# Kernel optimization log

Measured on AMD Instinct MI355X. Metric: run time of the kernel, lower is better.

Reference implementation:

```python
import jax, jax.numpy as jnp
import numpy as np

B, L, E = 4, 2048, 1024
H, D = E // 64, 64
FF = E // 4 * 11  # 2816

def _ln(x, g, b, eps=1e-5):
    m = jnp.mean(x, axis=-1, keepdims=True)
    v = jnp.mean((x - m) ** 2, axis=-1, keepdims=True)
    return (x - m) * jax.lax.rsqrt(v + eps) * g + b

def _fwd(x, g_norm, b_norm, W_ffn1, b_ffn1, W_ffn2, b_ffn2, g_head, b_head, mem,
         g_mem, b_mem, W_q, b_q, W_k, b_k, W_v, b_v, W_g, b_g, W_mg, b_mg,
         W_o, b_o, W_op, b_op, g_ctx, b_ctx, seq_dim):
    # Pre-norm + FFN (SiLU MLP), residual
    x_norm = _ln(x, g_norm, b_norm)
    x_mlp = x + jax.nn.silu(x_norm @ W_ffn1 + b_ffn1) @ W_ffn2 + b_ffn2
    # causal cumsum gating per head
    xc = jnp.cumsum(x_mlp, axis=seq_dim)
    x_h = x_mlp.reshape(B, L, H, D)
    xc_h = xc.reshape(B, L, H, D)
    align = jnp.sum(_ln(x_h, g_head, b_head) * _ln(xc_h, g_head, b_head),
                    axis=-1, keepdims=True) / (D ** 0.5)
    context = jnp.cumsum((x_h * jax.nn.sigmoid(align)).reshape(B, L, E), axis=seq_dim)
    # delta-rule fast-weight memory
    ctx = _ln(x_mlp + context, g_mem, b_mem)
    q = ctx @ W_q + b_q
    k = ctx @ W_k + b_k
    k = k / jnp.maximum(jnp.linalg.norm(k, axis=-1, keepdims=True), 1e-5)  # F.normalize
    v = ctx @ W_v + b_v
    gate = jax.nn.sigmoid(ctx @ W_g + b_g)
    prev = jnp.broadcast_to(mem, (B, E, E))
    scale = E ** 0.5
    v_ret = jnp.einsum('ble,bef->blf', k, prev) / scale
    v_dyn = gate * (v - v_ret)
    mem_out_prev = jnp.einsum('ble,bef->blf', q, prev)
    scores_causal = jnp.einsum('bld,bmd->blm', q, k) * jnp.tril(jnp.ones((L, L), q.dtype))
    mem_out = (mem_out_prev + jnp.einsum('blm,bmf->blf', scores_causal, v_dyn) / scale) / scale
    out = jax.nn.silu(mem_out @ W_o + b_o) @ W_op + b_op
    y = x_mlp + _ln(out, g_ctx, b_ctx)
    return y, scores_causal

def setup_inputs():
    key = jax.random.key(0)
    ks = jax.random.split(key, 12)
    w = lambda k, s: (jax.random.normal(k, s) * 0.02).astype(jnp.float32)
    z = lambda s: jnp.zeros(s, jnp.float32)
    o = lambda s: jnp.ones(s, jnp.float32)
    return {
        'x': jax.random.normal(ks[0], (B, L, E), jnp.float32),
        'g_norm': o((E,)), 'b_norm': z((E,)),
        'W_ffn1': w(ks[1], (E, FF)), 'b_ffn1': z((FF,)),
        'W_ffn2': w(ks[2], (FF, E)), 'b_ffn2': z((E,)),
        'g_head': o((D,)), 'b_head': z((D,)),
        'mem': w(ks[3], (1, E, E)),
        'g_mem': o((E,)), 'b_mem': z((E,)),
        'W_q': w(ks[4], (E, E)), 'b_q': z((E,)),
        'W_k': w(ks[5], (E, E)), 'b_k': z((E,)),
        'W_v': w(ks[6], (E, E)), 'b_v': z((E,)),
        'W_g': w(ks[7], (E, E)), 'b_g': z((E,)),
        'W_mg': w(ks[8], (E, E)), 'b_mg': z((E,)),
        'W_o': w(ks[9], (E, 4 * E)), 'b_o': z((4 * E,)),
        'W_op': w(ks[10], (4 * E, E)), 'b_op': z((E,)),
        'g_ctx': o((E,)), 'b_ctx': z((E,)),
        'seq_dim': 1,
    }

def reference(x, g_norm, b_norm, W_ffn1, b_ffn1, W_ffn2, b_ffn2, g_head, b_head, mem,
              g_mem, b_mem, W_q, b_q, W_k, b_k, W_v, b_v, W_g, b_g, W_mg, b_mg,
              W_o, b_o, W_op, b_op, g_ctx, b_ctx, seq_dim):
    return _fwd(x, g_norm, b_norm, W_ffn1, b_ffn1, W_ffn2, b_ffn2, g_head, b_head, mem,
                g_mem, b_mem, W_q, b_q, W_k, b_k, W_v, b_v, W_g, b_g, W_mg, b_mg,
                W_o, b_o, W_op, b_op, g_ctx, b_ctx, seq_dim)
```

## Files before the change

### kernel.cpp

```cpp
#include <hip/hip_runtime.h>
#include <math.h>

#define B_ 4
#define L_ 2048
#define E_ 1024
#define H_ 16
#define D_ 64
#define FF_ 2816
#define M_ (B_*L_)
#define E4_ 4096
#define CH_ 64
#define NC_ (L_/CH_)

typedef unsigned short ushort_t;
typedef __attribute__((ext_vector_type(8))) short short8;
typedef __attribute__((ext_vector_type(4))) float f32x4;
typedef __attribute__((ext_vector_type(4))) unsigned short ushort4v;

__device__ inline ushort_t f2b(float x) {
  union { float f; unsigned u; } v; v.f = x;
  unsigned r = v.u + 0x7FFFu + ((v.u >> 16) & 1u);
  return (ushort_t)(r >> 16);
}
__device__ inline float b2f(ushort_t h) {
  union { unsigned u; float f; } v; v.u = ((unsigned)h) << 16; return v.f;
}
__device__ inline void split8(const float* s, short8& hi, short8& lo) {
#pragma unroll
  for (int i = 0; i < 8; ++i) {
    unsigned u; { union { float f; unsigned x; } c; c.f = s[i]; u = c.x; }
    unsigned hu = u & 0xFFFF0000u;
    hi[i] = (short)(hu >> 16);
    union { unsigned x; float f; } hc; hc.x = hu;
    lo[i] = (short)f2b(s[i] - hc.f);
  }
}

__device__ inline float wave_sum(float a) {
#pragma unroll
  for (int off = 1; off < 64; off <<= 1) a += __shfl_xor(a, off);
  return a;
}
__device__ inline void wave_reduce2(float& a, float& b) {
#pragma unroll
  for (int off = 1; off < 64; off <<= 1) {
    a += __shfl_xor(a, off);
    b += __shfl_xor(b, off);
  }
}

__global__ __launch_bounds__(256) void ln_rows(
    const float* __restrict__ in, const float* __restrict__ g,
    const float* __restrict__ bb, const float* __restrict__ res_after,
    float* __restrict__ outf, ushort_t* __restrict__ outb,
    ushort_t* __restrict__ outbl)
{
  int row = blockIdx.x;
  int t = threadIdx.x;
  float4 v = ((const float4*)(in + (size_t)row * E_))[t];
  float s = wave_sum(v.x + v.y + v.z + v.w);
  __shared__ float ra[4], rb[4];
  int w = t >> 6;
  if ((t & 63) == 0) ra[w] = s;
  __syncthreads();
  float mean = (ra[0] + ra[1] + ra[2] + ra[3]) * (1.f / E_);
  float dx = v.x - mean, dy = v.y - mean, dz = v.z - mean, dw = v.w - mean;
  float s2 = wave_sum(dx*dx + dy*dy + dz*dz + dw*dw);
  if ((t & 63) == 0) rb[w] = s2;
  __syncthreads();
  float var = (rb[0] + rb[1] + rb[2] + rb[3]) * (1.f / E_);
  float r = rsqrtf(var + 1e-5f);
  float4 gv = ((const float4*)g)[t];
  float4 bv = ((const float4*)bb)[t];
  float4 o;
  o.x = dx * r * gv.x + bv.x;
  o.y = dy * r * gv.y + bv.y;
  o.z = dz * r * gv.z + bv.z;
  o.w = dw * r * gv.w + bv.w;
  if (res_after) {
    float4 rv = ((const float4*)(res_after + (size_t)row * E_))[t];
    o.x += rv.x; o.y += rv.y; o.z += rv.z; o.w += rv.w;
  }
  if (outf) ((float4*)(outf + (size_t)row * E_))[t] = o;
  if (outb) {
    ushort4v hb; hb.x = f2b(o.x); hb.y = f2b(o.y); hb.z = f2b(o.z); hb.w = f2b(o.w);
    *(ushort4v*)(outb + (size_t)row * E_ + t * 4) = hb;
    if (outbl) {
      ushort4v lb;
      lb.x = f2b(o.x - b2f(hb.x)); lb.y = f2b(o.y - b2f(hb.y));
      lb.z = f2b(o.z - b2f(hb.z)); lb.w = f2b(o.w - b2f(hb.w));
      *(ushort4v*)(outbl + (size_t)row * E_ + t * 4) = lb;
    }
  }
}

__global__ __launch_bounds__(256) void knorm_rows(
    const float* __restrict__ kin, ushort_t* __restrict__ kh,
    ushort_t* __restrict__ kl)
{
  int row = blockIdx.x;
  int t = threadIdx.x;
  float4 v = ((const float4*)(kin + (size_t)row * E_))[t];
  float s2 = wave_sum(v.x*v.x + v.y*v.y + v.z*v.z + v.w*v.w);
  __shared__ float rb2[4];
  int w = t >> 6;
  if ((t & 63) == 0) rb2[w] = s2;
  __syncthreads();
  s2 = rb2[0] + rb2[1] + rb2[2] + rb2[3];
  float sc = 1.f / fmaxf(sqrtf(s2), 1e-5f);
  float f0 = v.x * sc, f1 = v.y * sc, f2 = v.z * sc, f3 = v.w * sc;
  ushort4v hb; hb.x = f2b(f0); hb.y = f2b(f1); hb.z = f2b(f2); hb.w = f2b(f3);
  ushort4v lb;
  lb.x = f2b(f0 - b2f(hb.x)); lb.y = f2b(f1 - b2f(hb.y));
  lb.z = f2b(f2 - b2f(hb.z)); lb.w = f2b(f3 - b2f(hb.w));
  *(ushort4v*)(kh + (size_t)row * E_ + t * 4) = hb;
  *(ushort4v*)(kl + (size_t)row * E_ + t * 4) = lb;
}

__global__ __launch_bounds__(256) void chunk_partials(
    const float* __restrict__ x, float* __restrict__ S)
{
  int c = blockIdx.x, b = blockIdx.y, t = threadIdx.x;
  const float4* xp = (const float4*)(x + ((size_t)b * L_ + (size_t)c * CH_) * E_);
  float4 acc = make_float4(0.f, 0.f, 0.f, 0.f);
  for (int l = 0; l < CH_; ++l) {
    float4 v = xp[(size_t)l * (E_/4) + t];
    acc.x += v.x; acc.y += v.y; acc.z += v.z; acc.w += v.w;
  }
  ((float4*)(S + ((size_t)b * NC_ + c) * E_))[t] = acc;
}

__global__ __launch_bounds__(256) void scan_partials(float* __restrict__ S)
{
  int b = blockIdx.x, t = threadIdx.x;
  float4 run = make_float4(0.f, 0.f, 0.f, 0.f);
  for (int c = 0; c < NC_; ++c) {
    float4* p = (float4*)(S + ((size_t)b * NC_ + c) * E_);
    float4 v = p[t];
    p[t] = run;
    run.x += v.x; run.y += v.y; run.z += v.z; run.w += v.w;
  }
}

__global__ __launch_bounds__(64) void align_gate(
    const float* __restrict__ xmlp, const float* __restrict__ Sx,
    const float* __restrict__ gh, const float* __restrict__ bh,
    float* __restrict__ gated, float* __restrict__ G)
{
  int c = blockIdx.x, h = blockIdx.y, b = blockIdx.z;
  int d = threadIdx.x;
  int e = h * D_ + d;
  float xc = Sx[((size_t)b * NC_ + c) * E_ + e];
  float gsum = 0.f;
  float ghd = gh[d], bhd = bh[d];
  const float* xp = xmlp + ((size_t)b * L_ + (size_t)c * CH_) * E_ + e;
  float* gp = gated + ((size_t)b * L_ + (size_t)c * CH_) * E_ + e;
  for (int l = 0; l < CH_; ++l) {
    float xv = xp[(size_t)l * E_];
    xc += xv;
    float sx = xv, sc = xc;
    wave_reduce2(sx, sc);
    float mx = sx * (1.f/64.f), mc = sc * (1.f/64.f);
    float dx = xv - mx, dc = xc - mc;
    float vx = dx * dx, vc = dc * dc;
    wave_reduce2(vx, vc);
    vx *= (1.f/64.f); vc *= (1.f/64.f);
    float nx  = dx * rsqrtf(vx + 1e-5f) * ghd + bhd;
    float ncv = dc * rsqrtf(vc + 1e-5f) * ghd + bhd;
    float dotv = wave_sum(nx * ncv);
    float align = dotv * 0.125f;
    float sig = 1.f / (1.f + expf(-align));
    float gv = xv * sig;
    gp[(size_t)l * E_] = gv;
    gsum += gv;
  }
  G[((size_t)b * NC_ + c) * E_ + e] = gsum;
}

__global__ __launch_bounds__(256) void context_add(
    const float* __restrict__ gated, const float* __restrict__ Gx,
    const float* __restrict__ xmlp, float* __restrict__ t_out)
{
  int c = blockIdx.x, b = blockIdx.y, t = threadIdx.x;
  float4 run = ((const float4*)(Gx + ((size_t)b * NC_ + c) * E_))[t];
  size_t base = ((size_t)b * L_ + (size_t)c * CH_) * (E_/4);
  const float4* gp = (const float4*)gated;
  const float4* xp = (const float4*)xmlp;
  float4* op = (float4*)t_out;
  for (int l = 0; l < CH_; ++l) {
    size_t idx = base + (size_t)l * (E_/4) + t;
    float4 g = gp[idx];
    run.x += g.x; run.y += g.y; run.z += g.z; run.w += g.w;
    float4 x = xp[idx];
    float4 o;
    o.x = x.x + run.x; o.y = x.y + run.y; o.z = x.z + run.z; o.w = x.w + run.w;
    op[idx] = o;
  }
}

__global__ __launch_bounds__(256) void wcvt_t(
    const float* __restrict__ in, ushort_t* __restrict__ outh,
    ushort_t* __restrict__ outl, int R, int C)
{
  __shared__ float t[32][33];
  int c0 = blockIdx.x * 32, r0 = blockIdx.y * 32;
  int tid = threadIdx.x;
  int r = tid >> 3, c4 = (tid & 7) * 4;
  float4 v = *(const float4*)(in + (size_t)(r0 + r) * C + c0 + c4);
  t[r][c4] = v.x; t[r][c4+1] = v.y; t[r][c4+2] = v.z; t[r][c4+3] = v.w;
  __syncthreads();
  int c = tid >> 3, r4 = (tid & 7) * 4;
  float f0 = t[r4][c], f1 = t[r4+1][c], f2 = t[r4+2][c], f3 = t[r4+3][c];
  ushort4v hb; hb.x = f2b(f0); hb.y = f2b(f1); hb.z = f2b(f2); hb.w = f2b(f3);
  *(ushort4v*)(outh + (size_t)(c0 + c) * R + r0 + r4) = hb;
  if (outl) {
    ushort4v lb;
    lb.x = f2b(f0 - b2f(hb.x)); lb.y = f2b(f1 - b2f(hb.y));
    lb.z = f2b(f2 - b2f(hb.z)); lb.w = f2b(f3 - b2f(hb.w));
    *(ushort4v*)(outl + (size_t)(c0 + c) * R + r0 + r4) = lb;
  }
}

__global__ __launch_bounds__(256) void tpose_f32(
    const float* __restrict__ in, float* __restrict__ out)
{
  __shared__ float t[32][33];
  int b = blockIdx.z;
  const float* ib = in + (size_t)b * L_ * E_;
  float* ob = out + (size_t)b * E_ * L_;
  int c0 = blockIdx.x * 32, r0 = blockIdx.y * 32;
  int tid = threadIdx.x;
  int r = tid >> 3, c4 = (tid & 7) * 4;
  float4 v = *(const float4*)(ib + (size_t)(r0 + r) * E_ + c0 + c4);
  t[r][c4] = v.x; t[r][c4+1] = v.y; t[r][c4+2] = v.z; t[r][c4+3] = v.w;
  __syncthreads();
  int c = tid >> 3, r4 = (tid & 7) * 4;
  float4 o;
  o.x = t[r4][c]; o.y = t[r4+1][c]; o.z = t[r4+2][c]; o.w = t[r4+3][c];
  *(float4*)(ob + (size_t)(c0 + c) * L_ + r0 + r4) = o;
}

enum { EPI_PLAIN = 0, EPI_BIAS = 1, EPI_SILU = 2, EPI_SIG = 3,
       EPI_BIAS_RES = 4, EPI_VDYN = 5, EPI_PV = 6, EPI_TRIL = 7, EPI_RES = 8 };

struct GemmP {
  const ushort_t *A, *Al, *Bt, *Btl;
  const float *Af, *Btf;
  float* Cf; ushort_t *Cb, *Cbl;
  int N, K, ldA, ldB;
  long long sA, sB, sCf, sCb, sRes, sAux;
  const float *bias, *res, *aux;
  int epi, causal;
};

template <int MODE>
__global__ __launch_bounds__(256) void gemm_k(GemmP p)
{
  __shared__ __align__(16) short As[4][2][128][8];
  __shared__ __align__(16) short Bs[4][2][128][8];

  int z = blockIdx.z;
  int row0 = blockIdx.y * 128, col0 = blockIdx.x * 128;
  int tid = threadIdx.x;

  if (p.causal == 1 && col0 > row0) {
    float* Cf = p.Cf ? p.Cf + (size_t)z * p.sCf : nullptr;
    float4 zf = make_float4(0.f, 0.f, 0.f, 0.f);
#pragma unroll
    for (int i = 0; i < 16; ++i) {
      int e4 = tid + 256 * i;
      int r = e4 >> 5, c4 = (e4 & 31) * 4;
      if (Cf) *(float4*)(Cf + (size_t)(row0 + r) * p.N + col0 + c4) = zf;
    }
    return;
  }

  int lane = tid & 63, wave = tid >> 6;
  int wm = wave >> 1, wn = wave & 1;
  int lr = lane & 15, kq = lane >> 4;
  int lrx = lr ^ (kq << 1);

  int kend = p.K;
  if (p.causal == 2) { int ke = row0 + 128; kend = ke < p.K ? ke : p.K; }

  int kw = tid & 3, m0 = tid >> 2, m1 = m0 + 64;
  int sl0 = m0 ^ (kw << 1), sl1 = m1 ^ (kw << 1);

  size_t aoff0 = (size_t)(row0 + m0) * p.ldA + kw * 8;
  size_t aoff1 = (size_t)(row0 + m1) * p.ldA + kw * 8;
  size_t boff0 = (size_t)(col0 + m0) * p.ldB + kw * 8;
  size_t boff1 = (size_t)(col0 + m1) * p.ldB + kw * 8;

  const ushort_t *Ah = nullptr, *Bh = nullptr, *Alo = nullptr, *Blo = nullptr;
  const float *Af = nullptr, *Bf = nullptr;
  if constexpr (MODE == 2) {
    Af = p.Af  + (size_t)z * p.sA;
    Bf = p.Btf + (size_t)z * p.sB;
  } else {
    Ah = p.A  + (size_t)z * p.sA;
    Bh = p.Bt + (size_t)z * p.sB;
    if constexpr (MODE == 1) {
      Alo = p.Al  + (size_t)z * p.sA;
      Blo = p.Btl + (size_t)z * p.sB;
    }
  }

  f32x4 acc[4][4] = {};

  short8 a0h, a1h, b0h, b1h, a0l, a1l, b0l, b1l;
  float fa0[8], fa1[8], fb0[8], fb1[8];

  if constexpr (MODE == 2) {
    *(float4*)&fa0[0] = *(const float4*)(Af + aoff0);
    *(float4*)&fa0[4] = *(const float4*)(Af + aoff0 + 4);
    *(float4*)&fa1[0] = *(const float4*)(Af + aoff1);
    *(float4*)&fa1[4] = *(const float4*)(Af + aoff1 + 4);
    *(float4*)&fb0[0] = *(const float4*)(Bf + boff0);
    *(float4*)&fb0[4] = *(const float4*)(Bf + boff0 + 4);
    *(float4*)&fb1[0] = *(const float4*)(Bf + boff1);
    *(float4*)&fb1[4] = *(const float4*)(Bf + boff1 + 4);
  } else {
    a0h = *(const short8*)(Ah + aoff0);
    a1h = *(const short8*)(Ah + aoff1);
    b0h = *(const short8*)(Bh + boff0);
    b1h = *(const short8*)(Bh + boff1);
    if constexpr (MODE == 1) {
      a0l = *(const short8*)(Alo + aoff0);
      a1l = *(const short8*)(Alo + aoff1);
      b0l = *(const short8*)(Blo + boff0);
      b1l = *(const short8*)(Blo + boff1);
    }
  }

  for (int k0 = 0; k0 < kend; k0 += 32) {
    __syncthreads();
    if constexpr (MODE == 2) {
      split8(fa0, a0h, a0l); split8(fa1, a1h, a1l);
      split8(fb0, b0h, b0l); split8(fb1, b1h, b1l);
    }
    *(short8*)&As[kw][0][sl0][0] = a0h;
    *(short8*)&As[kw][0][sl1][0] = a1h;
    *(short8*)&Bs[kw][0][sl0][0] = b0h;
    *(short8*)&Bs[kw][0][sl1][0] = b1h;
    if constexpr (MODE != 0) {
      *(short8*)&As[kw][1][sl0][0] = a0l;
      *(short8*)&As[kw][1][sl1][0] = a1l;
      *(short8*)&Bs[kw][1][sl0][0] = b0l;
      *(short8*)&Bs[kw][1][sl1][0] = b1l;
    }
    __syncthreads();
    if (k0 + 32 < kend) {
      size_t kk = k0 + 32;
      if constexpr (MODE == 2) {
        *(float4*)&fa0[0] = *(const float4*)(Af + aoff0 + kk);
        *(float4*)&fa0[4] = *(const float4*)(Af + aoff0 + kk + 4);
        *(float4*)&fa1[0] = *(const float4*)(Af + aoff1 + kk);
        *(float4*)&fa1[4] = *(const float4*)(Af + aoff1 + kk + 4);
        *(float4*)&fb0[0] = *(const float4*)(Bf + boff0 + kk);
        *(float4*)&fb0[4] = *(const float4*)(Bf + boff0 + kk + 4);
        *(float4*)&fb1[0] = *(const float4*)(Bf + boff1 + kk);
        *(float4*)&fb1[4] = *(const float4*)(Bf + boff1 + kk + 4);
      } else {
        a0h = *(const short8*)(Ah + aoff0 + kk);
        a1h = *(const short8*)(Ah + aoff1 + kk);
        b0h = *(const short8*)(Bh + boff0 + kk);
        b1h = *(const short8*)(Bh + boff1 + kk);
        if constexpr (MODE == 1) {
          a0l = *(const short8*)(Alo + aoff0 + kk);
          a1l = *(const short8*)(Alo + aoff1 + kk);
          b0l = *(const short8*)(Blo + boff0 + kk);
          b1l = *(const short8*)(Blo + boff1 + kk);
        }
      }
    }
    short8 bh[4], bl[4];
#pragma unroll
    for (int ni = 0; ni < 4; ++ni) {
      bh[ni] = *(const short8*)&Bs[kq][0][wn * 64 + ni * 16 + lrx][0];
      if (MODE != 0) bl[ni] = *(const short8*)&Bs[kq][1][wn * 64 + ni * 16 + lrx][0];
    }
#pragma unroll
    for (int mi = 0; mi < 4; ++mi) {
      short8 ah = *(const short8*)&As[kq][0][wm * 64 + mi * 16 + lrx][0];
      short8 alv;
      if (MODE != 0) alv = *(const short8*)&As[kq][1][wm * 64 + mi * 16 + lrx][0];
#pragma unroll
      for (int ni = 0; ni < 4; ++ni) {
        acc[mi][ni] = __builtin_amdgcn_mfma_f32_16x16x32_bf16(
            ah, bh[ni], acc[mi][ni], 0, 0, 0);
        if (MODE != 0) {
          acc[mi][ni] = __builtin_amdgcn_mfma_f32_16x16x32_bf16(
              alv, bh[ni], acc[mi][ni], 0, 0, 0);
          acc[mi][ni] = __builtin_amdgcn_mfma_f32_16x16x32_bf16(
              ah, bl[ni], acc[mi][ni], 0, 0, 0);
        }
      }
    }
  }

  float* Cf = p.Cf ? p.Cf + (size_t)z * p.sCf : nullptr;
  ushort_t* Cb  = p.Cb  ? p.Cb  + (size_t)z * p.sCb : nullptr;
  ushort_t* Cbl = p.Cbl ? p.Cbl + (size_t)z * p.sCb : nullptr;
  const float* res = p.res ? p.res + (size_t)z * p.sRes : nullptr;
  const float* aux = p.aux ? p.aux + (size_t)z * p.sAux : nullptr;
  const float INV32 = 0.03125f;
  int rbase = kq * 4;

#pragma unroll
  for (int mi = 0; mi < 4; ++mi) {
#pragma unroll
    for (int r = 0; r < 4; ++r) {
      int grow = row0 + wm * 64 + mi * 16 + rbase + r;
      size_t rowoff = (size_t)grow * p.N;
#pragma unroll
      for (int ni = 0; ni < 4; ++ni) {
        int gcol = col0 + wn * 64 + ni * 16 + lr;
        size_t idx = rowoff + gcol;
        float v = acc[mi][ni][r];
        switch (p.epi) {
          case EPI_PLAIN: break;
          case EPI_BIAS: v += p.bias[gcol]; break;
          case EPI_SILU: v += p.bias[gcol]; v = v / (1.f + expf(-v)); break;
          case EPI_SIG:  v = 1.f / (1.f + expf(-(v + p.bias[gcol]))); break;
          case EPI_BIAS_RES: v += p.bias[gcol] + res[idx]; break;
          case EPI_VDYN: v = aux[idx] * (res[idx] - v * INV32); break;
          case EPI_PV:   v = (res[idx] + v * INV32) * INV32; break;
          case EPI_TRIL: v = (gcol <= grow) ? v : 0.f; break;
          case EPI_RES:  v += res[idx]; break;
        }
        if (Cf) Cf[idx] = v;
        if (Cb) {
          ushort_t hi = f2b(v);
          Cb[idx] = hi;
          if (Cbl) Cbl[idx] = f2b(v - b2f(hi));
        }
      }
    }
  }
}

struct GArgs {
  int mode;
  const ushort_t *A, *Al, *Bt, *Btl;
  const float *Af, *Btf;
  float* Cf; ushort_t *Cb, *Cbl;
  int M, N, K, ldA, ldB, nb;
  long long sA, sB, sCf, sCb, sRes, sAux;
  const float *bias, *res, *aux;
  int epi, causal;
};

static void launch_gemm(const GArgs& a, hipStream_t stream)
{
  GemmP p;
  p.A = a.A; p.Al = a.Al; p.Bt = a.Bt; p.Btl = a.Btl;
  p.Af = a.Af; p.Btf = a.Btf;
  p.Cf = a.Cf; p.Cb = a.Cb; p.Cbl = a.Cbl;
  p.N = a.N; p.K = a.K; p.ldA = a.ldA; p.ldB = a.ldB;
  p.sA = a.sA; p.sB = a.sB; p.sCf = a.sCf; p.sCb = a.sCb;
  p.sRes = a.sRes; p.sAux = a.sAux;
  p.bias = a.bias; p.res = a.res; p.aux = a.aux;
  p.epi = a.epi; p.causal = a.causal;
  dim3 grid(a.N / 128, a.M / 128, a.nb), blk(256);
  if (a.mode == 0)      gemm_k<0><<<grid, blk, 0, stream>>>(p);
  else if (a.mode == 1) gemm_k<1><<<grid, blk, 0, stream>>>(p);
  else                  gemm_k<2><<<grid, blk, 0, stream>>>(p);
}

extern "C" void kernel_launch(void* const* d_in, const int* in_sizes, int n_in,
                              void* d_out, int out_size, void* d_ws, size_t ws_size,
                              hipStream_t stream)
{
  const float* x      = (const float*)d_in[0];
  const float* g_norm = (const float*)d_in[1];
  const float* b_norm = (const float*)d_in[2];
  const float* W1     = (const float*)d_in[3];
  const float* b1     = (const float*)d_in[4];
  const float* W2     = (const float*)d_in[5];
  const float* b2     = (const float*)d_in[6];
  const float* g_head = (const float*)d_in[7];
  const float* b_head = (const float*)d_in[8];
  const float* memW   = (const float*)d_in[9];
  const float* g_mem  = (const float*)d_in[10];
  const float* b_mem  = (const float*)d_in[11];
  const float* W_q    = (const float*)d_in[12];
  const float* b_q    = (const float*)d_in[13];
  const float* W_k    = (const float*)d_in[14];
  const float* b_k    = (const float*)d_in[15];
  const float* W_v    = (const float*)d_in[16];
  const float* b_v    = (const float*)d_in[17];
  const float* W_g    = (const float*)d_in[18];
  const float* b_g    = (const float*)d_in[19];
  const float* W_o    = (const float*)d_in[22];
  const float* b_o    = (const float*)d_in[23];
  const float* W_op   = (const float*)d_in[24];
  const float* b_op   = (const float*)d_in[25];
  const float* g_ctx  = (const float*)d_in[26];
  const float* b_ctx  = (const float*)d_in[27];

  float* out = (float*)d_out;
  char* w = (char*)d_ws;
  auto alloc = [&](size_t bytes) { char* p = w; w += (bytes + 255) & ~(size_t)255; return p; };

  const size_t ME  = (size_t)M_ * E_;
  const size_t EE  = (size_t)E_ * E_;
  const size_t E4E = (size_t)E_ * E4_;

  ushort_t* W1t  = (ushort_t*)alloc((size_t)FF_ * E_ * 2);
  ushort_t* W2t  = (ushort_t*)alloc((size_t)E_ * FF_ * 2);
  ushort_t* Wqt  = (ushort_t*)alloc(2 * EE * 2);
  ushort_t* Wkt  = (ushort_t*)alloc(2 * EE * 2);
  ushort_t* Wvt  = (ushort_t*)alloc(2 * EE * 2);
  ushort_t* Wgt  = (ushort_t*)alloc(2 * EE * 2);
  ushort_t* memT = (ushort_t*)alloc(2 * EE * 2);
  ushort_t* Wot  = (ushort_t*)alloc(2 * E4E * 2);
  ushort_t* Wopt = (ushort_t*)alloc(2 * E4E * 2);
  float* P0 = (float*)alloc(ME * 4);
  float* P1 = (float*)alloc(ME * 4);
  float* P2 = (float*)alloc(ME * 4);
  ushort_t* Q1 = (ushort_t*)alloc(2 * ME * 2);
  ushort_t* Q2 = (ushort_t*)alloc(2 * ME * 2);
  ushort_t* Q3 = (ushort_t*)alloc(2 * ME * 2);
  ushort_t* SH = (ushort_t*)alloc((size_t)M_ * FF_ * 2);
  float* Sb = (float*)alloc((size_t)B_ * NC_ * E_ * 4);
  float* Gb = (float*)alloc((size_t)B_ * NC_ * E_ * 4);
  if ((size_t)(w - (char*)d_ws) > ws_size) return;

  float* y_out  = out;
  float* sc_out = out + ME;

  wcvt_t<<<dim3(FF_/32, E_/32),  256, 0, stream>>>(W1,   W1t,  nullptr,    E_,  FF_);
  wcvt_t<<<dim3(E_/32,  FF_/32), 256, 0, stream>>>(W2,   W2t,  nullptr,    FF_, E_);
  wcvt_t<<<dim3(E_/32,  E_/32),  256, 0, stream>>>(W_q,  Wqt,  Wqt + EE,   E_,  E_);
  wcvt_t<<<dim3(E_/32,  E_/32),  256, 0, stream>>>(W_k,  Wkt,  Wkt + EE,   E_,  E_);
  wcvt_t<<<dim3(E_/32,  E_/32),  256, 0, stream>>>(W_v,  Wvt,  Wvt + EE,   E_,  E_);
  wcvt_t<<<dim3(E_/32,  E_/32),  256, 0, stream>>>(W_g,  Wgt,  Wgt + EE,   E_,  E_);
  wcvt_t<<<dim3(E_/32,  E_/32),  256, 0, stream>>>(memW, memT, memT + EE,  E_,  E_);
  wcvt_t<<<dim3(E4_/32, E_/32),  256, 0, stream>>>(W_o,  Wot,  Wot + E4E,  E_,  E4_);
  wcvt_t<<<dim3(E_/32,  E4_/32), 256, 0, stream>>>(W_op, Wopt, Wopt + E4E, E4_, E_);

  GArgs g{};

  ln_rows<<<M_, 256, 0, stream>>>(x, g_norm, b_norm, nullptr, nullptr, Q1, nullptr);
  g = GArgs(); g.mode = 0; g.A = Q1; g.Bt = W1t; g.Cb = SH;
  g.M = M_; g.N = FF_; g.K = E_; g.ldA = E_; g.ldB = E_; g.nb = 1;
  g.bias = b1; g.epi = EPI_SILU; launch_gemm(g, stream);
  g = GArgs(); g.mode = 0; g.A = SH; g.Bt = W2t; g.Cf = P0;
  g.M = M_; g.N = E_; g.K = FF_; g.ldA = FF_; g.ldB = FF_; g.nb = 1;
  g.bias = b2; g.res = x; g.epi = EPI_BIAS_RES; launch_gemm(g, stream);
  chunk_partials<<<dim3(NC_, B_), 256, 0, stream>>>(P0, Sb);
  scan_partials<<<B_, 256, 0, stream>>>(Sb);
  align_gate<<<dim3(NC_, H_, B_), 64, 0, stream>>>(P0, Sb, g_head, b_head, P1, Gb);
  scan_partials<<<B_, 256, 0, stream>>>(Gb);
  context_add<<<dim3(NC_, B_), 256, 0, stream>>>(P1, Gb, P0, P2);
  ln_rows<<<M_, 256, 0, stream>>>(P2, g_mem, b_mem, nullptr, nullptr, Q1, Q1 + ME);
  g = GArgs(); g.mode = 1; g.A = Q1; g.Al = Q1 + ME; g.Bt = Wqt; g.Btl = Wqt + EE;
  g.Cb = Q2; g.Cbl = Q2 + ME; g.M = M_; g.N = E_; g.K = E_; g.ldA = E_; g.ldB = E_;
  g.nb = 1; g.bias = b_q; g.epi = EPI_BIAS; launch_gemm(g, stream);
  g.Bt = Wkt; g.Btl = Wkt + EE; g.Cb = nullptr; g.Cbl = nullptr; g.Cf = P1;
  g.bias = b_k; launch_gemm(g, stream);
  knorm_rows<<<M_, 256, 0, stream>>>(P1, Q3, Q3 + ME);
  g.Bt = Wvt; g.Btl = Wvt + EE; g.Cf = P1; g.bias = b_v; launch_gemm(g, stream);
  g.Bt = Wgt; g.Btl = Wgt + EE; g.Cf = P2; g.bias = b_g; g.epi = EPI_SIG;
  launch_gemm(g, stream);
  g = GArgs(); g.mode = 1; g.A = Q3; g.Al = Q3 + ME; g.Bt = memT; g.Btl = memT + EE;
  g.Cf = (float*)Q1; g.M = M_; g.N = E_; g.K = E_; g.ldA = E_; g.ldB = E_; g.nb = 1;
  g.res = P1; g.aux = P2; g.epi = EPI_VDYN; launch_gemm(g, stream);
  tpose_f32<<<dim3(E_/32, L_/32, B_), 256, 0, stream>>>((float*)Q1, P1);
  g = GArgs(); g.mode = 1; g.A = Q2; g.Al = Q2 + ME; g.Bt = Q3; g.Btl = Q3 + ME;
  g.Cf = sc_out; g.M = L_; g.N = L_; g.K = E_; g.ldA = E_; g.ldB = E_; g.nb = B_;
  g.sA = (long long)L_ * E_; g.sB = (long long)L_ * E_; g.sCf = (long long)L_ * L_;
  g.epi = EPI_TRIL; g.causal = 1; launch_gemm(g, stream);
  g = GArgs(); g.mode = 1; g.A = Q2; g.Al = Q2 + ME; g.Bt = memT; g.Btl = memT + EE;
  g.Cf = P2; g.M = M_; g.N = E_; g.K = E_; g.ldA = E_; g.ldB = E_; g.nb = 1;
  g.epi = EPI_PLAIN; launch_gemm(g, stream);
  g = GArgs(); g.mode = 2; g.Af = sc_out; g.Btf = P1;
  g.Cb = Q2; g.Cbl = Q2 + ME; g.M = L_; g.N = E_; g.K = L_; g.ldA = L_; g.ldB = L_;
  g.nb = B_; g.sA = (long long)L_ * L_; g.sB = (long long)E_ * L_;
  g.sCb = (long long)L_ * E_; g.sRes = (long long)L_ * E_;
  g.res = P2; g.epi = EPI_PV; g.causal = 2; launch_gemm(g, stream);
  const size_t SHLO = (size_t)M_ * 1024;
  for (int c = 0; c < 4; ++c) {
    g = GArgs(); g.mode = 1; g.A = Q2; g.Al = Q2 + ME;
    g.Bt = Wot + (size_t)c * 1024 * E_; g.Btl = Wot + E4E + (size_t)c * 1024 * E_;
    g.Cb = SH; g.Cbl = SH + SHLO;
    g.M = M_; g.N = 1024; g.K = E_; g.ldA = E_; g.ldB = E_; g.nb = 1;
    g.bias = b_o + c * 1024; g.epi = EPI_SILU; launch_gemm(g, stream);
    g = GArgs(); g.mode = 1; g.A = SH; g.Al = SH + SHLO;
    g.Bt = Wopt + (size_t)c * 1024; g.Btl = Wopt + E4E + (size_t)c * 1024;
    g.M = M_; g.N = E_; g.K = 1024; g.ldA = 1024; g.ldB = E4_; g.nb = 1;
    if (c == 0) { g.Cf = P1; g.epi = EPI_PLAIN; }
    else if (c < 3) { g.Cf = P1; g.res = P1; g.epi = EPI_RES; }
    else { g.Cf = P2; g.res = P1; g.bias = b_op; g.epi = EPI_BIAS_RES; }
    launch_gemm(g, stream);
  }
  ln_rows<<<M_, 256, 0, stream>>>(P2, g_ctx, b_ctx, P0, y_out, nullptr, nullptr);
}
```

Measured before the change: 1.603 ms.

## Use direct global-to-LDS loads, fuse QKVG GEMM, precompute split bf16 operands

The GEMM kernel now stages tiles with global_load_lds straight into shared memory and drops the register prefetch path. The q/k/v/gate projections become one GEMM over N=4096 with a per-column-group epilogue. The fp32 split mode is removed: the scores GEMM writes hi/lo bf16 copies and the transpose emits split bf16, so the PV GEMM no longer splits in its inner loop. The output MLP is chunked in two halves instead of four. This cuts launches and inner-loop conversion work, but loses register-level prefetch overlap and writes extra bf16 score buffers.

```diff
diff --git a/kernel.cpp b/kernel.cpp
--- a/kernel.cpp
+++ b/kernel.cpp
@@ -25,15 +25,11 @@
 __device__ inline float b2f(ushort_t h) {
   union { unsigned u; float f; } v; v.u = ((unsigned)h) << 16; return v.f;
 }
-__device__ inline void split8(const float* s, short8& hi, short8& lo) {
-#pragma unroll
-  for (int i = 0; i < 8; ++i) {
-    unsigned u; { union { float f; unsigned x; } c; c.f = s[i]; u = c.x; }
-    unsigned hu = u & 0xFFFF0000u;
-    hi[i] = (short)(hu >> 16);
-    union { unsigned x; float f; } hc; hc.x = hu;
-    lo[i] = (short)f2b(s[i] - hc.f);
-  }
+
+__device__ inline void gload16(const void* g, void* l) {
+  __builtin_amdgcn_global_load_lds(
+      (__attribute__((address_space(1))) void*)(g),
+      (__attribute__((address_space(3))) void*)(l), 16, 0, 0);
 }
 
 __device__ inline float wave_sum(float a) {
@@ -221,13 +217,14 @@
   }
 }
 
-__global__ __launch_bounds__(256) void tpose_f32(
-    const float* __restrict__ in, float* __restrict__ out)
+__global__ __launch_bounds__(256) void tpose_f2p(
+    const float* __restrict__ in, ushort_t* __restrict__ outh,
+    ushort_t* __restrict__ outl)
 {
   __shared__ float t[32][33];
   int b = blockIdx.z;
   const float* ib = in + (size_t)b * L_ * E_;
-  float* ob = out + (size_t)b * E_ * L_;
+  size_t ob = (size_t)b * E_ * L_;
   int c0 = blockIdx.x * 32, r0 = blockIdx.y * 32;
   int tid = threadIdx.x;
   int r = tid >> 3, c4 = (tid & 7) * 4;
@@ -235,29 +232,36 @@
   t[r][c4] = v.x; t[r][c4+1] = v.y; t[r][c4+2] = v.z; t[r][c4+3] = v.w;
   __syncthreads();
   int c = tid >> 3, r4 = (tid & 7) * 4;
-  float4 o;
-  o.x = t[r4][c]; o.y = t[r4+1][c]; o.z = t[r4+2][c]; o.w = t[r4+3][c];
-  *(float4*)(ob + (size_t)(c0 + c) * L_ + r0 + r4) = o;
+  float f0 = t[r4][c], f1 = t[r4+1][c], f2 = t[r4+2][c], f3 = t[r4+3][c];
+  ushort4v hb; hb.x = f2b(f0); hb.y = f2b(f1); hb.z = f2b(f2); hb.w = f2b(f3);
+  ushort4v lb;
+  lb.x = f2b(f0 - b2f(hb.x)); lb.y = f2b(f1 - b2f(hb.y));
+  lb.z = f2b(f2 - b2f(hb.z)); lb.w = f2b(f3 - b2f(hb.w));
+  size_t oidx = ob + (size_t)(c0 + c) * L_ + r0 + r4;
+  *(ushort4v*)(outh + oidx) = hb;
+  *(ushort4v*)(outl + oidx) = lb;
 }
 
 enum { EPI_PLAIN = 0, EPI_BIAS = 1, EPI_SILU = 2, EPI_SIG = 3,
-       EPI_BIAS_RES = 4, EPI_VDYN = 5, EPI_PV = 6, EPI_TRIL = 7, EPI_RES = 8 };
+       EPI_BIAS_RES = 4, EPI_VDYN = 5, EPI_PV = 6, EPI_TRIL = 7,
+       EPI_QKVG = 9 };
 
 struct GemmP {
   const ushort_t *A, *Al, *Bt, *Btl;
-  const float *Af, *Btf;
-  float* Cf; ushort_t *Cb, *Cbl;
+  float *Cf, *Cf2, *Cf3;
+  ushort_t *Cb, *Cbl;
   int N, K, ldA, ldB;
-  long long sA, sB, sCf, sCb, sRes, sAux;
-  const float *bias, *res, *aux;
+  long long sA, sB, sCf, sCb, sRes;
+  const float *bias, *bias1, *bias2, *bias3, *res, *aux;
   int epi, causal;
 };
 
 template <int MODE>
 __global__ __launch_bounds__(256) void gemm_k(GemmP p)
 {
-  __shared__ __align__(16) short As[4][2][128][8];
-  __shared__ __align__(16) short Bs[4][2][128][8];
+  constexpr int NP = (MODE == 1) ? 2 : 1;
+  __shared__ __align__(16) short As[NP][4][128][8];
+  __shared__ __align__(16) short Bs[NP][4][128][8];
 
   int z = blockIdx.z;
   int row0 = blockIdx.y * 128, col0 = blockIdx.x * 128;
@@ -265,132 +269,89 @@
 
   if (p.causal == 1 && col0 > row0) {
     float* Cf = p.Cf ? p.Cf + (size_t)z * p.sCf : nullptr;
+    ushort_t* Cb  = p.Cb  ? p.Cb  + (size_t)z * p.sCb : nullptr;
+    ushort_t* Cbl = p.Cbl ? p.Cbl + (size_t)z * p.sCb : nullptr;
     float4 zf = make_float4(0.f, 0.f, 0.f, 0.f);
+    ushort4v zb = {0, 0, 0, 0};
 #pragma unroll
     for (int i = 0; i < 16; ++i) {
       int e4 = tid + 256 * i;
       int r = e4 >> 5, c4 = (e4 & 31) * 4;
-      if (Cf) *(float4*)(Cf + (size_t)(row0 + r) * p.N + col0 + c4) = zf;
+      size_t idx = (size_t)(row0 + r) * p.N + col0 + c4;
+      if (Cf)  *(float4*)(Cf + idx) = zf;
+      if (Cb)  *(ushort4v*)(Cb + idx) = zb;
+      if (Cbl) *(ushort4v*)(Cbl + idx) = zb;
     }
     return;
   }
 
-  int lane = tid & 63, wave = tid >> 6;
-  int wm = wave >> 1, wn = wave & 1;
+  const ushort_t* Ah = p.A  + (size_t)z * p.sA;
+  const ushort_t* Bh = p.Bt + (size_t)z * p.sB;
+  const ushort_t* Alo = nullptr; const ushort_t* Blo = nullptr;
+  if constexpr (MODE == 1) {
+    Alo = p.Al  + (size_t)z * p.sA;
+    Blo = p.Btl + (size_t)z * p.sB;
+  }
+
+  int lane = tid & 63, wv = tid >> 6;
+  int wm = wv >> 1, wn = wv & 1;
   int lr = lane & 15, kq = lane >> 4;
   int lrx = lr ^ (kq << 1);
 
   int kend = p.K;
   if (p.causal == 2) { int ke = row0 + 128; kend = ke < p.K ? ke : p.K; }
 
-  int kw = tid & 3, m0 = tid >> 2, m1 = m0 + 64;
-  int sl0 = m0 ^ (kw << 1), sl1 = m1 ^ (kw << 1);
-
-  size_t aoff0 = (size_t)(row0 + m0) * p.ldA + kw * 8;
-  size_t aoff1 = (size_t)(row0 + m1) * p.ldA + kw * 8;
-  size_t boff0 = (size_t)(col0 + m0) * p.ldB + kw * 8;
-  size_t boff1 = (size_t)(col0 + m1) * p.ldB + kw * 8;
-
-  const ushort_t *Ah = nullptr, *Bh = nullptr, *Alo = nullptr, *Blo = nullptr;
-  const float *Af = nullptr, *Bf = nullptr;
-  if constexpr (MODE == 2) {
-    Af = p.Af  + (size_t)z * p.sA;
-    Bf = p.Btf + (size_t)z * p.sB;
-  } else {
-    Ah = p.A  + (size_t)z * p.sA;
-    Bh = p.Bt + (size_t)z * p.sB;
-    if constexpr (MODE == 1) {
-      Alo = p.Al  + (size_t)z * p.sA;
-      Blo = p.Btl + (size_t)z * p.sB;
-    }
-  }
+  int c2i = tid + 256;
+  int kw1 = tid >> 7, m1 = (tid & 127) ^ (kw1 << 1);
+  int kw2 = c2i >> 7, m2 = (c2i & 127) ^ (kw2 << 1);
+  size_t aof1 = (size_t)(row0 + m1) * p.ldA + kw1 * 8;
+  size_t aof2 = (size_t)(row0 + m2) * p.ldA + kw2 * 8;
+  size_t bof1 = (size_t)(col0 + m1) * p.ldB + kw1 * 8;
+  size_t bof2 = (size_t)(col0 + m2) * p.ldB + kw2 * 8;
+
+  short* a0 = &As[0][0][0][0];
+  short* b0 = &Bs[0][0][0][0];
+  short* lA1 = a0 + wv * 512;
+  short* lA2 = a0 + 2048 + wv * 512;
+  short* lB1 = b0 + wv * 512;
+  short* lB2 = b0 + 2048 + wv * 512;
 
   f32x4 acc[4][4] = {};
-
-  short8 a0h, a1h, b0h, b1h, a0l, a1l, b0l, b1l;
-  float fa0[8], fa1[8], fb0[8], fb1[8];
-
-  if constexpr (MODE == 2) {
-    *(float4*)&fa0[0] = *(const float4*)(Af + aoff0);
-    *(float4*)&fa0[4] = *(const float4*)(Af + aoff0 + 4);
-    *(float4*)&fa1[0] = *(const float4*)(Af + aoff1);
-    *(float4*)&fa1[4] = *(const float4*)(Af + aoff1 + 4);
-    *(float4*)&fb0[0] = *(const float4*)(Bf + boff0);
-    *(float4*)&fb0[4] = *(const float4*)(Bf + boff0 + 4);
-    *(float4*)&fb1[0] = *(const float4*)(Bf + boff1);
-    *(float4*)&fb1[4] = *(const float4*)(Bf + boff1 + 4);
-  } else {
-    a0h = *(const short8*)(Ah + aoff0);
-    a1h = *(const short8*)(Ah + aoff1);
-    b0h = *(const short8*)(Bh + boff0);
-    b1h = *(const short8*)(Bh + boff1);
-    if constexpr (MODE == 1) {
-      a0l = *(const short8*)(Alo + aoff0);
-      a1l = *(const short8*)(Alo + aoff1);
-      b0l = *(const short8*)(Blo + boff0);
-      b1l = *(const short8*)(Blo + boff1);
-    }
-  }
 
   for (int k0 = 0; k0 < kend; k0 += 32) {
     __syncthreads();
-    if constexpr (MODE == 2) {
-      split8(fa0, a0h, a0l); split8(fa1, a1h, a1l);
-      split8(fb0, b0h, b0l); split8(fb1, b1h, b1l);
-    }
-    *(short8*)&As[kw][0][sl0][0] = a0h;
-    *(short8*)&As[kw][0][sl1][0] = a1h;
-    *(short8*)&Bs[kw][0][sl0][0] = b0h;
-    *(short8*)&Bs[kw][0][sl1][0] = b1h;
-    if constexpr (MODE != 0) {
-      *(short8*)&As[kw][1][sl0][0] = a0l;
-      *(short8*)&As[kw][1][sl1][0] = a1l;
-      *(short8*)&Bs[kw][1][sl0][0] = b0l;
-      *(short8*)&Bs[kw][1][sl1][0] = b1l;
+    gload16(Ah + aof1 + k0, lA1);
+    gload16(Ah + aof2 + k0, lA2);
+    gload16(Bh + bof1 + k0, lB1);
+    gload16(Bh + bof2 + k0, lB2);
+    if constexpr (MODE == 1) {
+      gload16(Alo + aof1 + k0, a0 + 4096 + wv * 512);
+      gload16(Alo + aof2 + k0, a0 + 6144 + wv * 512);
+      gload16(Blo + bof1 + k0, b0 + 4096 + wv * 512);
+      gload16(Blo + bof2 + k0, b0 + 6144 + wv * 512);
     }
     __syncthreads();
-    if (k0 + 32 < kend) {
-      size_t kk = k0 + 32;
-      if constexpr (MODE == 2) {
-        *(float4*)&fa0[0] = *(const float4*)(Af + aoff0 + kk);
-        *(float4*)&fa0[4] = *(const float4*)(Af + aoff0 + kk + 4);
-        *(float4*)&fa1[0] = *(const float4*)(Af + aoff1 + kk);
-        *(float4*)&fa1[4] = *(const float4*)(Af + aoff1 + kk + 4);
-        *(float4*)&fb0[0] = *(const float4*)(Bf + boff0 + kk);
-        *(float4*)&fb0[4] = *(const float4*)(Bf + boff0 + kk + 4);
-        *(float4*)&fb1[0] = *(const float4*)(Bf + boff1 + kk);
-        *(float4*)&fb1[4] = *(const float4*)(Bf + boff1 + kk + 4);
-      } else {
-        a0h = *(const short8*)(Ah + aoff0 + kk);
-        a1h = *(const short8*)(Ah + aoff1 + kk);
-        b0h = *(const short8*)(Bh + boff0 + kk);
-        b1h = *(const short8*)(Bh + boff1 + kk);
-        if constexpr (MODE == 1) {
-          a0l = *(const short8*)(Alo + aoff0 + kk);
-          a1l = *(const short8*)(Alo + aoff1 + kk);
-          b0l = *(const short8*)(Blo + boff0 + kk);
-          b1l = *(const short8*)(Blo + boff1 + kk);
-        }
-      }
-    }
+
     short8 bh[4], bl[4];
 #pragma unroll
     for (int ni = 0; ni < 4; ++ni) {
-      bh[ni] = *(const short8*)&Bs[kq][0][wn * 64 + ni * 16 + lrx][0];
-      if (MODE != 0) bl[ni] = *(const short8*)&Bs[kq][1][wn * 64 + ni * 16 + lrx][0];
+      bh[ni] = *(const short8*)&Bs[0][kq][wn * 64 + ni * 16 + lrx][0];
+      if constexpr (MODE == 1)
+        bl[ni] = *(const short8*)&Bs[NP-1][kq][wn * 64 + ni * 16 + lrx][0];
     }
 #pragma unroll
     for (int mi = 0; mi < 4; ++mi) {
-      short8 ah = *(const short8*)&As[kq][0][wm * 64 + mi * 16 + lrx][0];
-      short8 alv;
-      if (MODE != 0) alv = *(const short8*)&As[kq][1][wm * 64 + mi * 16 + lrx][0];
+      short8 ah = *(const short8*)&As[0][kq][wm * 64 + mi * 16 + lrx][0];
+      short8 al;
+      if constexpr (MODE == 1)
+        al = *(const short8*)&As[NP-1][kq][wm * 64 + mi * 16 + lrx][0];
 #pragma unroll
       for (int ni = 0; ni < 4; ++ni) {
         acc[mi][ni] = __builtin_amdgcn_mfma_f32_16x16x32_bf16(
             ah, bh[ni], acc[mi][ni], 0, 0, 0);
-        if (MODE != 0) {
+        if constexpr (MODE == 1) {
           acc[mi][ni] = __builtin_amdgcn_mfma_f32_16x16x32_bf16(
-              alv, bh[ni], acc[mi][ni], 0, 0, 0);
+              al, bh[ni], acc[mi][ni], 0, 0, 0);
           acc[mi][ni] = __builtin_amdgcn_mfma_f32_16x16x32_bf16(
               ah, bl[ni], acc[mi][ni], 0, 0, 0);
         }
@@ -398,13 +359,42 @@
     }
   }
 
+  int rbase = kq * 4;
+  const float INV32 = 0.03125f;
+
+  if (p.epi == EPI_QKVG) {
+    int gi = col0 >> 10;
+    int cb0 = col0 & 1023;
+    const float* gb = gi == 0 ? p.bias : gi == 1 ? p.bias1
+                    : gi == 2 ? p.bias2 : p.bias3;
+#pragma unroll
+    for (int mi = 0; mi < 4; ++mi) {
+#pragma unroll
+      for (int r = 0; r < 4; ++r) {
+        int grow = row0 + wm * 64 + mi * 16 + rbase + r;
+        size_t rowoff = (size_t)grow * 1024;
+#pragma unroll
+        for (int ni = 0; ni < 4; ++ni) {
+          int gc = cb0 + wn * 64 + ni * 16 + lr;
+          size_t idx = rowoff + gc;
+          float v = acc[mi][ni][r] + gb[gc];
+          if (gi == 0) {
+            ushort_t hi = f2b(v);
+            p.Cb[idx] = hi;
+            p.Cbl[idx] = f2b(v - b2f(hi));
+          } else if (gi == 1) p.Cf[idx] = v;
+          else if (gi == 2) p.Cf2[idx] = v;
+          else p.Cf3[idx] = 1.f / (1.f + expf(-v));
+        }
+      }
+    }
+    return;
+  }
+
   float* Cf = p.Cf ? p.Cf + (size_t)z * p.sCf : nullptr;
   ushort_t* Cb  = p.Cb  ? p.Cb  + (size_t)z * p.sCb : nullptr;
   ushort_t* Cbl = p.Cbl ? p.Cbl + (size_t)z * p.sCb : nullptr;
   const float* res = p.res ? p.res + (size_t)z * p.sRes : nullptr;
-  const float* aux = p.aux ? p.aux + (size_t)z * p.sAux : nullptr;
-  const float INV32 = 0.03125f;
-  int rbase = kq * 4;
 
 #pragma unroll
   for (int mi = 0; mi < 4; ++mi) {
@@ -423,10 +413,9 @@
           case EPI_SILU: v += p.bias[gcol]; v = v / (1.f + expf(-v)); break;
           case EPI_SIG:  v = 1.f / (1.f + expf(-(v + p.bias[gcol]))); break;
           case EPI_BIAS_RES: v += p.bias[gcol] + res[idx]; break;
-          case EPI_VDYN: v = aux[idx] * (res[idx] - v * INV32); break;
+          case EPI_VDYN: v = p.aux[idx] * (res[idx] - v * INV32); break;
           case EPI_PV:   v = (res[idx] + v * INV32) * INV32; break;
           case EPI_TRIL: v = (gcol <= grow) ? v : 0.f; break;
-          case EPI_RES:  v += res[idx]; break;
         }
         if (Cf) Cf[idx] = v;
         if (Cb) {
@@ -439,32 +428,11 @@
   }
 }
 
-struct GArgs {
-  int mode;
-  const ushort_t *A, *Al, *Bt, *Btl;
-  const float *Af, *Btf;
-  float* Cf; ushort_t *Cb, *Cbl;
-  int M, N, K, ldA, ldB, nb;
-  long long sA, sB, sCf, sCb, sRes, sAux;
-  const float *bias, *res, *aux;
-  int epi, causal;
-};
-
-static void launch_gemm(const GArgs& a, hipStream_t stream)
-{
-  GemmP p;
-  p.A = a.A; p.Al = a.Al; p.Bt = a.Bt; p.Btl = a.Btl;
-  p.Af = a.Af; p.Btf = a.Btf;
-  p.Cf = a.Cf; p.Cb = a.Cb; p.Cbl = a.Cbl;
-  p.N = a.N; p.K = a.K; p.ldA = a.ldA; p.ldB = a.ldB;
-  p.sA = a.sA; p.sB = a.sB; p.sCf = a.sCf; p.sCb = a.sCb;
-  p.sRes = a.sRes; p.sAux = a.sAux;
-  p.bias = a.bias; p.res = a.res; p.aux = a.aux;
-  p.epi = a.epi; p.causal = a.causal;
-  dim3 grid(a.N / 128, a.M / 128, a.nb), blk(256);
-  if (a.mode == 0)      gemm_k<0><<<grid, blk, 0, stream>>>(p);
-  else if (a.mode == 1) gemm_k<1><<<grid, blk, 0, stream>>>(p);
-  else                  gemm_k<2><<<grid, blk, 0, stream>>>(p);
+static void run_gemm(const GemmP& p, int M, int nb, int mode, hipStream_t s)
+{
+  dim3 grid(p.N / 128, M / 128, nb), blk(256);
+  if (mode == 0) gemm_k<0><<<grid, blk, 0, s>>>(p);
+  else           gemm_k<1><<<grid, blk, 0, s>>>(p);
 }
 
 extern "C" void kernel_launch(void* const* d_in, const int* in_sizes, int n_in,
@@ -505,13 +473,11 @@
   const size_t ME  = (size_t)M_ * E_;
   const size_t EE  = (size_t)E_ * E_;
   const size_t E4E = (size_t)E_ * E4_;
+  const size_t BLL = (size_t)B_ * L_ * L_;
 
   ushort_t* W1t  = (ushort_t*)alloc((size_t)FF_ * E_ * 2);
   ushort_t* W2t  = (ushort_t*)alloc((size_t)E_ * FF_ * 2);
-  ushort_t* Wqt  = (ushort_t*)alloc(2 * EE * 2);
-  ushort_t* Wkt  = (ushort_t*)alloc(2 * EE * 2);
-  ushort_t* Wvt  = (ushort_t*)alloc(2 * EE * 2);
-  ushort_t* Wgt  = (ushort_t*)alloc(2 * EE * 2);
+  ushort_t* W4   = (ushort_t*)alloc(8 * EE * 2);
   ushort_t* memT = (ushort_t*)alloc(2 * EE * 2);
   ushort_t* Wot  = (ushort_t*)alloc(2 * E4E * 2);
   ushort_t* Wopt = (ushort_t*)alloc(2 * E4E * 2);
@@ -521,78 +487,87 @@
   ushort_t* Q1 = (ushort_t*)alloc(2 * ME * 2);
   ushort_t* Q2 = (ushort_t*)alloc(2 * ME * 2);
   ushort_t* Q3 = (ushort_t*)alloc(2 * ME * 2);
-  ushort_t* SH = (ushort_t*)alloc((size_t)M_ * FF_ * 2);
+  ushort_t* SH = (ushort_t*)alloc(2 * BLL * 2);
   float* Sb = (float*)alloc((size_t)B_ * NC_ * E_ * 4);
   float* Gb = (float*)alloc((size_t)B_ * NC_ * E_ * 4);
   if ((size_t)(w - (char*)d_ws) > ws_size) return;
 
   float* y_out  = out;
   float* sc_out = out + ME;
-
-  wcvt_t<<<dim3(FF_/32, E_/32),  256, 0, stream>>>(W1,   W1t,  nullptr,    E_,  FF_);
-  wcvt_t<<<dim3(E_/32,  FF_/32), 256, 0, stream>>>(W2,   W2t,  nullptr,    FF_, E_);
-  wcvt_t<<<dim3(E_/32,  E_/32),  256, 0, stream>>>(W_q,  Wqt,  Wqt + EE,   E_,  E_);
-  wcvt_t<<<dim3(E_/32,  E_/32),  256, 0, stream>>>(W_k,  Wkt,  Wkt + EE,   E_,  E_);
-  wcvt_t<<<dim3(E_/32,  E_/32),  256, 0, stream>>>(W_v,  Wvt,  Wvt + EE,   E_,  E_);
-  wcvt_t<<<dim3(E_/32,  E_/32),  256, 0, stream>>>(W_g,  Wgt,  Wgt + EE,   E_,  E_);
-  wcvt_t<<<dim3(E_/32,  E_/32),  256, 0, stream>>>(memW, memT, memT + EE,  E_,  E_);
-  wcvt_t<<<dim3(E4_/32, E_/32),  256, 0, stream>>>(W_o,  Wot,  Wot + E4E,  E_,  E4_);
-  wcvt_t<<<dim3(E_/32,  E4_/32), 256, 0, stream>>>(W_op, Wopt, Wopt + E4E, E4_, E_);
-
-  GArgs g{};
+  ushort_t* P2u = (ushort_t*)P2;
+  float* gateF  = (float*)SH;
+
+  wcvt_t<<<dim3(FF_/32, E_/32),  256, 0, stream>>>(W1,   W1t,  nullptr,        E_,  FF_);
+  wcvt_t<<<dim3(E_/32,  FF_/32), 256, 0, stream>>>(W2,   W2t,  nullptr,        FF_, E_);
+  wcvt_t<<<dim3(E_/32,  E_/32),  256, 0, stream>>>(W_q,  W4,        W4 + 4*EE,       E_, E_);
+  wcvt_t<<<dim3(E_/32,  E_/32),  256, 0, stream>>>(W_k,  W4 + EE,   W4 + 5*EE,       E_, E_);
+  wcvt_t<<<dim3(E_/32,  E_/32),  256, 0, stream>>>(W_v,  W4 + 2*EE, W4 + 6*EE,       E_, E_);
+  wcvt_t<<<dim3(E_/32,  E_/32),  256, 0, stream>>>(W_g,  W4 + 3*EE, W4 + 7*EE,       E_, E_);
+  wcvt_t<<<dim3(E_/32,  E_/32),  256, 0, stream>>>(memW, memT, memT + EE,      E_,  E_);
+  wcvt_t<<<dim3(E4_/32, E_/32),  256, 0, stream>>>(W_o,  Wot,  Wot + E4E,      E_,  E4_);
+  wcvt_t<<<dim3(E_/32,  E4_/32), 256, 0, stream>>>(W_op, Wopt, Wopt + E4E,     E4_, E_);
+
+  GemmP p{};
 
   ln_rows<<<M_, 256, 0, stream>>>(x, g_norm, b_norm, nullptr, nullptr, Q1, nullptr);
-  g = GArgs(); g.mode = 0; g.A = Q1; g.Bt = W1t; g.Cb = SH;
-  g.M = M_; g.N = FF_; g.K = E_; g.ldA = E_; g.ldB = E_; g.nb = 1;
-  g.bias = b1; g.epi = EPI_SILU; launch_gemm(g, stream);
-  g = GArgs(); g.mode = 0; g.A = SH; g.Bt = W2t; g.Cf = P0;
-  g.M = M_; g.N = E_; g.K = FF_; g.ldA = FF_; g.ldB = FF_; g.nb = 1;
-  g.bias = b2; g.res = x; g.epi = EPI_BIAS_RES; launch_gemm(g, stream);
+  p = GemmP{}; p.A = Q1; p.Bt = W1t; p.Cb = SH;
+  p.N = FF_; p.K = E_; p.ldA = E_; p.ldB = E_;
+  p.bias = b1; p.epi = EPI_SILU;
+  run_gemm(p, M_, 1, 0, stream);
+  p = GemmP{}; p.A = SH; p.Bt = W2t; p.Cf = P0;
+  p.N = E_; p.K = FF_; p.ldA = FF_; p.ldB = FF_;
+  p.bias = b2; p.res = x; p.epi = EPI_BIAS_RES;
+  run_gemm(p, M_, 1, 0, stream);
   chunk_partials<<<dim3(NC_, B_), 256, 0, stream>>>(P0, Sb);
   scan_partials<<<B_, 256, 0, stream>>>(Sb);
   align_gate<<<dim3(NC_, H_, B_), 64, 0, stream>>>(P0, Sb, g_head, b_head, P1, Gb);
   scan_partials<<<B_, 256, 0, stream>>>(Gb);
   context_add<<<dim3(NC_, B_), 256, 0, stream>>>(P1, Gb, P0, P2);
   ln_rows<<<M_, 256, 0, stream>>>(P2, g_mem, b_mem, nullptr, nullptr, Q1, Q1 + ME);
-  g = GArgs(); g.mode = 1; g.A = Q1; g.Al = Q1 + ME; g.Bt = Wqt; g.Btl = Wqt + EE;
-  g.Cb = Q2; g.Cbl = Q2 + ME; g.M = M_; g.N = E_; g.K = E_; g.ldA = E_; g.ldB = E_;
-  g.nb = 1; g.bias = b_q; g.epi = EPI_BIAS; launch_gemm(g, stream);
-  g.Bt = Wkt; g.Btl = Wkt + EE; g.Cb = nullptr; g.Cbl = nullptr; g.Cf = P1;
-  g.bias = b_k; launch_gemm(g, stream);
+  p = GemmP{}; p.A = Q1; p.Al = Q1 + ME; p.Bt = W4; p.Btl = W4 + 4*EE;
+  p.N = E4_; p.K = E_; p.ldA = E_; p.ldB = E_;
+  p.Cb = Q2; p.Cbl = Q2 + ME; p.Cf = P1; p.Cf2 = P2; p.Cf3 = gateF;
+  p.bias = b_q; p.bias1 = b_k; p.bias2 = b_v; p.bias3 = b_g;
+  p.epi = EPI_QKVG;
+  run_gemm(p, M_, 1, 1, stream);
   knorm_rows<<<M_, 256, 0, stream>>>(P1, Q3, Q3 + ME);
-  g.Bt = Wvt; g.Btl = Wvt + EE; g.Cf = P1; g.bias = b_v; launch_gemm(g, stream);
-  g.Bt = Wgt; g.Btl = Wgt + EE; g.Cf = P2; g.bias = b_g; g.epi = EPI_SIG;
-  launch_gemm(g, stream);
-  g = GArgs(); g.mode = 1; g.A = Q3; g.Al = Q3 + ME; g.Bt = memT; g.Btl = memT + EE;
-  g.Cf = (float*)Q1; g.M = M_; g.N = E_; g.K = E_; g.ldA = E_; g.ldB = E_; g.nb = 1;
-  g.res = P1; g.aux = P2; g.epi = EPI_VDYN; launch_gemm(g, stream);
-  tpose_f32<<<dim3(E_/32, L_/32, B_), 256, 0, stream>>>((float*)Q1, P1);
-  g = GArgs(); g.mode = 1; g.A = Q2; g.Al = Q2 + ME; g.Bt = Q3; g.Btl = Q3 + ME;
-  g.Cf = sc_out; g.M = L_; g.N = L_; g.K = E_; g.ldA = E_; g.ldB = E_; g.nb = B_;
-  g.sA = (long long)L_ * E_; g.sB = (long long)L_ * E_; g.sCf = (long long)L_ * L_;
-  g.epi = EPI_TRIL; g.causal = 1; launch_gemm(g, stream);
-  g = GArgs(); g.mode = 1; g.A = Q2; g.Al = Q2 + ME; g.Bt = memT; g.Btl = memT + EE;
-  g.Cf = P2; g.M = M_; g.N = E_; g.K = E_; g.ldA = E_; g.ldB = E_; g.nb = 1;
-  g.epi = EPI_PLAIN; launch_gemm(g, stream);
-  g = GArgs(); g.mode = 2; g.Af = sc_out; g.Btf = P1;
-  g.Cb = Q2; g.Cbl = Q2 + ME; g.M = L_; g.N = E_; g.K = L_; g.ldA = L_; g.ldB = L_;
-  g.nb = B_; g.sA = (long long)L_ * L_; g.sB = (long long)E_ * L_;
-  g.sCb = (long long)L_ * E_; g.sRes = (long long)L_ * E_;
-  g.res = P2; g.epi = EPI_PV; g.causal = 2; launch_gemm(g, stream);
-  const size_t SHLO = (size_t)M_ * 1024;
-  for (int c = 0; c < 4; ++c) {
-    g = GArgs(); g.mode = 1; g.A = Q2; g.Al = Q2 + ME;
-    g.Bt = Wot + (size_t)c * 1024 * E_; g.Btl = Wot + E4E + (size_t)c * 1024 * E_;
-    g.Cb = SH; g.Cbl = SH + SHLO;
-    g.M = M_; g.N = 1024; g.K = E_; g.ldA = E_; g.ldB = E_; g.nb = 1;
-    g.bias = b_o + c * 1024; g.epi = EPI_SILU; launch_gemm(g, stream);
-    g = GArgs(); g.mode = 1; g.A = SH; g.Al = SH + SHLO;
-    g.Bt = Wopt + (size_t)c * 1024; g.Btl = Wopt + E4E + (size_t)c * 1024;
-    g.M = M_; g.N = E_; g.K = 1024; g.ldA = 1024; g.ldB = E4_; g.nb = 1;
-    if (c == 0) { g.Cf = P1; g.epi = EPI_PLAIN; }
-    else if (c < 3) { g.Cf = P1; g.res = P1; g.epi = EPI_RES; }
-    else { g.Cf = P2; g.res = P1; g.bias = b_op; g.epi = EPI_BIAS_RES; }
-    launch_gemm(g, stream);
-  }
-  ln_rows<<<M_, 256, 0, stream>>>(P2, g_ctx, b_ctx, P0, y_out, nullptr, nullptr);
-}
+  p = GemmP{}; p.A = Q3; p.Al = Q3 + ME; p.Bt = memT; p.Btl = memT + EE;
+  p.N = E_; p.K = E_; p.ldA = E_; p.ldB = E_;
+  p.Cf = P1; p.res = P2; p.aux = gateF; p.epi = EPI_VDYN;
+  run_gemm(p, M_, 1, 1, stream);
+  tpose_f2p<<<dim3(E_/32, L_/32, B_), 256, 0, stream>>>(P1, P2u, P2u + ME);
+  p = GemmP{}; p.A = Q2; p.Al = Q2 + ME; p.Bt = Q3; p.Btl = Q3 + ME;
+  p.N = L_; p.K = E_; p.ldA = E_; p.ldB = E_;
+  p.sA = (long long)L_ * E_; p.sB = (long long)L_ * E_;
+  p.Cf = sc_out; p.sCf = (long long)L_ * L_;
+  p.Cb = SH; p.Cbl = SH + BLL; p.sCb = (long long)L_ * L_;
+  p.epi = EPI_TRIL; p.causal = 1;
+  run_gemm(p, L_, B_, 1, stream);
+  p = GemmP{}; p.A = Q2; p.Al = Q2 + ME; p.Bt = memT; p.Btl = memT + EE;
+  p.N = E_; p.K = E_; p.ldA = E_; p.ldB = E_;
+  p.Cf = P1; p.epi = EPI_PLAIN;
+  run_gemm(p, M_, 1, 1, stream);
+  p = GemmP{}; p.A = SH; p.Al = SH + BLL; p.Bt = P2u; p.Btl = P2u + ME;
+  p.N = E_; p.K = L_; p.ldA = L_; p.ldB = L_;
+  p.sA = (long long)L_ * L_; p.sB = (long long)E_ * L_;
+  p.Cb = Q1; p.Cbl = Q1 + ME; p.sCb = (long long)L_ * E_;
+  p.res = P1; p.sRes = (long long)L_ * E_;
+  p.epi = EPI_PV; p.causal = 2;
+  run_gemm(p, L_, B_, 1, stream);
+  const size_t SHLO = (size_t)M_ * 2048;
+  for (int c = 0; c < 2; ++c) {
+    p = GemmP{}; p.A = Q1; p.Al = Q1 + ME;
+    p.Bt = Wot + (size_t)c * 2048 * E_; p.Btl = Wot + E4E + (size_t)c * 2048 * E_;
+    p.N = 2048; p.K = E_; p.ldA = E_; p.ldB = E_;
+    p.Cb = SH; p.Cbl = SH + SHLO;
+    p.bias = b_o + c * 2048; p.epi = EPI_SILU;
+    run_gemm(p, M_, 1, 1, stream);
+    p = GemmP{}; p.A = SH; p.Al = SH + SHLO;
+    p.Bt = Wopt + (size_t)c * 2048; p.Btl = Wopt + E4E + (size_t)c * 2048;
+    p.N = E_; p.K = 2048; p.ldA = 2048; p.ldB = E4_;
+    if (c == 0) { p.Cf = P2; p.epi = EPI_PLAIN; }
+    else { p.Cf = P1; p.res = P2; p.bias = b_op; p.epi = EPI_BIAS_RES; }
+    run_gemm(p, M_, 1, 1, stream);
+  }
+  ln_rows<<<M_, 256, 0, stream>>>(P1, g_ctx, b_ctx, P0, y_out, nullptr, nullptr);
+}
```

After: 2.066 ms. 28.9% more time.
